# Optimization experiments

Measured on AMD Instinct MI355X. Metric: run time of the kernel, lower is better.

The kernel has to match this reference:

```python
import jax, jax.numpy as jnp
import numpy as np

N_HEADS = 4
HEAD_DIM = 64
NEG_SLOPE = 0.2
TIME_PE_DIM = 16


def time_pe(date):
    # TimePositionalEncoding: sin/cos features; 8 sin + 8 cos == pe_dim (16), no projection needed
    t = date.astype(jnp.float32) / 10000.0
    div = jnp.exp(jnp.arange(0, TIME_PE_DIM, 2, dtype=jnp.float32) * (-jnp.log(10000.0) / TIME_PE_DIM))
    arg = t[:, None] * div[None, :]  # [N, 8]
    return jnp.concatenate([jnp.sin(arg), jnp.cos(arg)], axis=-1)  # [N, 16]


def pearl_pe(x, edge_index, Wp, bp):
    # PEARL positional embedding approximated as mean-neighbor aggregation over the
    # union of all relations followed by a learned linear + tanh -> [N, 32]
    N = x.shape[0]
    src = edge_index[:, 0, :].reshape(-1)
    dst = edge_index[:, 1, :].reshape(-1)
    agg = jax.ops.segment_sum(x[src], dst, num_segments=N)
    deg = jax.ops.segment_sum(jnp.ones_like(dst, jnp.float32), dst, num_segments=N)
    agg = agg / jnp.maximum(deg, 1.0)[:, None]
    return jnp.tanh(agg @ Wp + bp)


def gatv2(x, src, dst, Wl, Wr, att, b):
    # GATv2 message passing for one edge type; dropout is identity (eval mode)
    N = x.shape[0]
    xl = (x @ Wl).reshape(N, N_HEADS, HEAD_DIM)
    xr = (x @ Wr).reshape(N, N_HEADS, HEAD_DIM)
    m = xl[src] + xr[dst]                                   # [E, H, C]
    e = jnp.sum(jax.nn.leaky_relu(m, NEG_SLOPE) * att, -1)  # [E, H]
    emax = jax.ops.segment_max(e, dst, num_segments=N)
    emax = jnp.where(jnp.isfinite(emax), emax, 0.0)
    ex = jnp.exp(e - emax[dst])
    denom = jax.ops.segment_sum(ex, dst, num_segments=N)
    alpha = ex / (denom[dst] + 1e-16)                       # segment softmax over in-edges
    out = jax.ops.segment_sum(xl[src] * alpha[..., None], dst, num_segments=N)
    return out.reshape(N, N_HEADS * HEAD_DIM) + b


def rel_agg(h_rel, W, b, a):
    # attention-weighted combination across relation outputs: h_rel [N, R, hidden]
    s = jnp.einsum('nrh,h->nr', jnp.tanh(h_rel @ W + b), a)
    w = jax.nn.softmax(s, axis=-1)
    return jnp.einsum('nr,nrh->nh', w, h_rel)


def gnn_layer(h, edge_index, Wl, Wr, att, b, aW, ab, aa):
    R = edge_index.shape[0]
    # HeteroConv aggr='sum': sum GATv2 outputs across the 5 relations
    conv_sum = gatv2(h, edge_index[0, 0], edge_index[0, 1], Wl[0], Wr[0], att[0], b[0])
    for r in range(1, R):
        conv_sum = conv_sum + gatv2(h, edge_index[r, 0], edge_index[r, 1], Wl[r], Wr[r], att[r], b[r])
    # original forward feeds conv_output['stock'] for every relation key (identical copies)
    h_rel = jnp.broadcast_to(conv_sum[:, None, :], (conv_sum.shape[0], R, conv_sum.shape[1]))
    h = rel_agg(h_rel, aW, ab, aa)
    return jax.nn.relu(h)  # dropout identity in eval


def reference(x, date_tensor, edge_index, pearl_W, pearl_b, Wl0, Wr0, att0, b0,
              Wl1, Wr1, att1, b1, aggW, aggb, agga, out_W1, out_b1, out_W2, out_b2):
    pe = pearl_pe(x, edge_index, pearl_W, pearl_b)          # [N, 32]
    tpe = time_pe(date_tensor)                              # [N, 16]
    h = jnp.concatenate([x, pe, tpe], axis=1)               # [N, 112]
    h = gnn_layer(h, edge_index, Wl0, Wr0, att0, b0, aggW[0], aggb[0], agga[0])
    h = gnn_layer(h, edge_index, Wl1, Wr1, att1, b1, aggW[1], aggb[1], agga[1])
    h = jax.nn.relu(h @ out_W1 + out_b1)
    return h @ out_W2 + out_b2                              # [N, 3]


def setup_inputs():
    key = jax.random.key(0)
    ks = jax.random.split(key, 20)
    N, E, R = 20000, 320000, 5
    IN, PE, HID = 64, 32, 256
    IN0 = IN + PE + TIME_PE_DIM  # 112

    def nrm(k, shp, sc=0.05):
        return jax.random.normal(k, shp, jnp.float32) * sc

    return {
        'x': jax.random.normal(ks[0], (N, IN), jnp.float32),
        'date_tensor': jax.random.randint(ks[1], (N,), 0, 20000, jnp.int32),
        'edge_index': jax.random.randint(ks[2], (R, 2, E), 0, N, jnp.int32),
        'pearl_W': nrm(ks[3], (IN, PE)),
        'pearl_b': jnp.zeros((PE,), jnp.float32),
        'Wl0': nrm(ks[4], (R, IN0, HID)),
        'Wr0': nrm(ks[5], (R, IN0, HID)),
        'att0': nrm(ks[6], (R, N_HEADS, HEAD_DIM)),
        'b0': jnp.zeros((R, HID), jnp.float32),
        'Wl1': nrm(ks[7], (R, HID, HID)),
        'Wr1': nrm(ks[8], (R, HID, HID)),
        'att1': nrm(ks[9], (R, N_HEADS, HEAD_DIM)),
        'b1': jnp.zeros((R, HID), jnp.float32),
        'aggW': nrm(ks[10], (2, HID, HID)),
        'aggb': jnp.zeros((2, HID), jnp.float32),
        'agga': nrm(ks[11], (2, HID)),
        'out_W1': nrm(ks[12], (HID, HID // 2)),
        'out_b1': jnp.zeros((HID // 2,), jnp.float32),
        'out_W2': nrm(ks[13], (HID // 2, 3)),
        'out_b2': jnp.zeros((3,), jnp.float32),
    }
```

## Files before the change

kernel.cpp:

```cpp
#include <hip/hip_runtime.h>
#include <math.h>

typedef __bf16 bf16x8 __attribute__((ext_vector_type(8)));
typedef float f32x4 __attribute__((ext_vector_type(4)));
typedef unsigned short u16x8 __attribute__((ext_vector_type(8)));

#define GLD16(src, dst)                                                        \
    __builtin_amdgcn_global_load_lds(                                          \
        (const __attribute__((address_space(1))) void*)(src),                  \
        (__attribute__((address_space(3))) void*)(dst), 16, 0, 0)

__device__ inline float bf2f(unsigned short u) {
    union { unsigned int i; float f; } c;
    c.i = ((unsigned int)u) << 16;
    return c.f;
}

template <int CTRL>
__device__ inline float dpp_add(float v) {
    int s = __builtin_amdgcn_update_dpp(0, __builtin_bit_cast(int, v), CTRL, 0xF, 0xF, true);
    return v + __builtin_bit_cast(float, s);
}


__global__ __launch_bounds__(256) void count_kernel(const int* __restrict__ ei,
                                                    int* __restrict__ cnt, int N, int E) {
    int idx = blockIdx.x * 256 + threadIdx.x;
    if (idx >= 5 * E) return;
    int r = idx / E;
    int e = idx - r * E;
    int dst = ei[(size_t)r * 2 * E + E + e];
    atomicAdd(&cnt[r * N + dst], 1);
}

__global__ __launch_bounds__(256) void scanA_kernel(const int* __restrict__ cnt,
                                                    int* __restrict__ off,
                                                    int* __restrict__ csums, int N, int NC) {
    int r = blockIdx.y, c = blockIdx.x, t = threadIdx.x;
    int idx0 = c * 1024 + t * 4;
    int v0 = (idx0 + 0 < N) ? cnt[r * N + idx0 + 0] : 0;
    int v1 = (idx0 + 1 < N) ? cnt[r * N + idx0 + 1] : 0;
    int v2 = (idx0 + 2 < N) ? cnt[r * N + idx0 + 2] : 0;
    int v3 = (idx0 + 3 < N) ? cnt[r * N + idx0 + 3] : 0;
    int ts = v0 + v1 + v2 + v3;
    __shared__ int sd[256];
    sd[t] = ts;
    __syncthreads();
    for (int s = 1; s < 256; s <<= 1) {
        int add = (t >= s) ? sd[t - s] : 0;
        __syncthreads();
        sd[t] += add;
        __syncthreads();
    }
    int excl = sd[t] - ts;
    size_t base = (size_t)r * (N + 1);
    if (idx0 + 0 < N) off[base + idx0 + 0] = excl;
    if (idx0 + 1 < N) off[base + idx0 + 1] = excl + v0;
    if (idx0 + 2 < N) off[base + idx0 + 2] = excl + v0 + v1;
    if (idx0 + 3 < N) off[base + idx0 + 3] = excl + v0 + v1 + v2;
    if (t == 255) csums[r * NC + c] = sd[255];
}

__global__ __launch_bounds__(64) void scanB_kernel(int* __restrict__ csums,
                                                   int* __restrict__ off, int N, int NC) {
    int r = threadIdx.x;
    if (r < 5) {
        int run = 0;
        for (int c = 0; c < NC; c++) {
            int t = csums[r * NC + c];
            csums[r * NC + c] = run;
            run += t;
        }
        off[(size_t)r * (N + 1) + N] = run;
    }
}

__global__ __launch_bounds__(256) void scanC_kernel(int* __restrict__ off,
                                                    const int* __restrict__ csums,
                                                    int* __restrict__ cur,
                                                    int N, int NC) {
    int r = blockIdx.y, c = blockIdx.x, t = threadIdx.x;
    int add = csums[r * NC + c];
    int idx0 = c * 1024 + t * 4;
    size_t base = (size_t)r * (N + 1);
#pragma unroll
    for (int j = 0; j < 4; j++)
        if (idx0 + j < N) {
            int v = off[base + idx0 + j] + add;
            off[base + idx0 + j] = v;
            cur[r * N + idx0 + j] = v;
        }
}

__global__ __launch_bounds__(256) void scatter_kernel(const int* __restrict__ ei,
                                                      int* __restrict__ cur,
                                                      unsigned short* __restrict__ srcs,
                                                      int N, int E) {
    int idx = blockIdx.x * 256 + threadIdx.x;
    if (idx >= 5 * E) return;
    int r = idx / E;
    int e = idx - r * E;
    int src = ei[(size_t)r * 2 * E + e];
    int dst = ei[(size_t)r * 2 * E + E + e];
    int pos = atomicAdd(&cur[r * N + dst], 1);
    srcs[(size_t)r * E + pos] = (unsigned short)src;
}


__global__ __launch_bounds__(256) void xcvt_kernel(const float* __restrict__ x,
                                                   unsigned short* __restrict__ xb, int total) {
    int idx = (blockIdx.x * 256 + threadIdx.x) * 4;
    if (idx >= total) return;
    float4 v = *(const float4*)(x + idx);
    __bf16 b0 = (__bf16)v.x, b1 = (__bf16)v.y, b2 = (__bf16)v.z, b3 = (__bf16)v.w;
    unsigned short* p = xb + idx;
    p[0] = *(unsigned short*)&b0;
    p[1] = *(unsigned short*)&b1;
    p[2] = *(unsigned short*)&b2;
    p[3] = *(unsigned short*)&b3;
}


__global__ __launch_bounds__(256) void pearl_h0_kernel(
    const float* __restrict__ x, const unsigned short* __restrict__ xb,
    const int* __restrict__ date,
    const int* __restrict__ off, const unsigned short* __restrict__ srcs,
    const float* __restrict__ pW, const float* __restrict__ pb,
    float* __restrict__ h0, int N, int E) {
    int lane = threadIdx.x & 63;
    int wid = blockIdx.x * 4 + (threadIdx.x >> 6);
    if (wid >= N) return;
    int n = __builtin_amdgcn_readfirstlane(wid);

    float acc = 0.f;
    int deg = 0;
    for (int r = 0; r < 5; r++) {
        int kb = off[(size_t)r * (N + 1) + n];
        int ke = off[(size_t)r * (N + 1) + n + 1];
        deg += ke - kb;
        const unsigned short* sp = srcs + (size_t)r * E;
        int k = kb;
        for (; k + 8 <= ke; k += 8) {
            int i0 = sp[k], i1 = sp[k + 1], i2 = sp[k + 2], i3 = sp[k + 3];
            int i4 = sp[k + 4], i5 = sp[k + 5], i6 = sp[k + 6], i7 = sp[k + 7];
            float a0 = bf2f(xb[(size_t)i0 * 64 + lane]);
            float a1 = bf2f(xb[(size_t)i1 * 64 + lane]);
            float a2 = bf2f(xb[(size_t)i2 * 64 + lane]);
            float a3 = bf2f(xb[(size_t)i3 * 64 + lane]);
            float a4 = bf2f(xb[(size_t)i4 * 64 + lane]);
            float a5 = bf2f(xb[(size_t)i5 * 64 + lane]);
            float a6 = bf2f(xb[(size_t)i6 * 64 + lane]);
            float a7 = bf2f(xb[(size_t)i7 * 64 + lane]);
            acc += ((a0 + a1) + (a2 + a3)) + ((a4 + a5) + (a6 + a7));
        }
        for (; k < ke; k++) acc += bf2f(xb[(size_t)sp[k] * 64 + lane]);
    }
    float an = acc / fmaxf((float)deg, 1.0f);

    float s = (lane < 32) ? pb[lane] : 0.f;
#pragma unroll 8
    for (int c = 0; c < 64; c++) {
        float av = __shfl(an, c, 64);
        if (lane < 32) s = fmaf(av, pW[c * 32 + lane], s);
    }

    h0[(size_t)n * 112 + lane] = x[(size_t)n * 64 + lane];
    if (lane < 32) h0[(size_t)n * 112 + 64 + lane] = tanhf(s);
    if (lane < 16) {
        float t = (float)date[n] / 10000.0f;
        int i = lane & 7;
        float dv = expf((float)(2 * i) * (-0.57564627324851148f));
        float arg = t * dv;
        h0[(size_t)n * 112 + 96 + lane] = (lane < 8) ? sinf(arg) : cosf(arg);
    }
}


__global__ __launch_bounds__(256) void pack_a_kernel(
    const float* __restrict__ A, __bf16* __restrict__ Ah, __bf16* __restrict__ Al,
    int M, int K, int Mp, int KT) {
    int KG = KT * 4;
    int idx = blockIdx.x * 256 + threadIdx.x;
    if (idx >= Mp * KG) return;
    int m = idx / KG, kgg = idx - m * KG;
    int kt = kgg >> 2, kg = kgg & 3;
    int k0 = kt * 32 + kg * 8;
    int mt = m >> 4, mr = m & 15;
    size_t out = (((size_t)mt * KT + kt) * 64 + kg * 16 + mr) * 8;
    bf16x8 hv, lv;
#pragma unroll
    for (int j = 0; j < 8; j++) {
        int k = k0 + j;
        float v = (m < M && k < K) ? A[(size_t)m * K + k] : 0.f;
        __bf16 h = (__bf16)v;
        hv[j] = h;
        lv[j] = (__bf16)(v - (float)h);
    }
    *(bf16x8*)(Ah + out) = hv;
    *(bf16x8*)(Al + out) = lv;
}


__global__ __launch_bounds__(256) void pack_w_kernel(
    const float* __restrict__ Wl0, const float* __restrict__ Wr0,
    const float* __restrict__ Wl1, const float* __restrict__ Wr1,
    const float* __restrict__ W1,
    __bf16* __restrict__ Wph, __bf16* __restrict__ Wpl) {
    const int S0 = 32768, S1 = 65536;
    int t = blockIdx.y;
    const float* W;
    int K, Nc, KT;
    size_t dst;
    if (t < 5)       { W = Wl0 + (size_t)t * 112 * 256;        K = 112; Nc = 256; KT = 4; dst = (size_t)t * S0; }
    else if (t < 10) { W = Wr0 + (size_t)(t - 5) * 112 * 256;  K = 112; Nc = 256; KT = 4; dst = 163840 + (size_t)(t - 5) * S0; }
    else if (t < 15) { W = Wl1 + (size_t)(t - 10) * 256 * 256; K = 256; Nc = 256; KT = 8; dst = 327680 + (size_t)(t - 10) * S1; }
    else if (t < 20) { W = Wr1 + (size_t)(t - 15) * 256 * 256; K = 256; Nc = 256; KT = 8; dst = 655360 + (size_t)(t - 15) * S1; }
    else             { W = W1;                                  K = 256; Nc = 128; KT = 8; dst = 983040; }
    int entries = (Nc / 16) * KT * 64;
    int idx = blockIdx.x * 256 + threadIdx.x;
    if (idx >= entries) return;
    int nt = idx / (KT * 64);
    int rem = idx - nt * (KT * 64);
    int kt = rem >> 6, lane = rem & 63;
    int kg = lane >> 4, nr = lane & 15;
    bf16x8 hv, lv;
#pragma unroll
    for (int j = 0; j < 8; j++) {
        int k = kt * 32 + kg * 8 + j;
        float v = (k < K) ? W[(size_t)k * Nc + nt * 16 + nr] : 0.f;
        __bf16 h = (__bf16)v;
        hv[j] = h;
        lv[j] = (__bf16)(v - (float)h);
    }
    *(bf16x8*)(Wph + dst + (size_t)idx * 8) = hv;
    *(bf16x8*)(Wpl + dst + (size_t)idx * 8) = lv;
}


__global__ __launch_bounds__(256) void gemm_mfma(
    const __bf16* __restrict__ Ah, const __bf16* __restrict__ Al,
    const __bf16* __restrict__ WLh, const __bf16* __restrict__ WLl,
    const __bf16* __restrict__ WRh, const __bf16* __restrict__ WRl,
    size_t strideB, void* __restrict__ Cl, void* __restrict__ Cr, size_t CstrideBytes,
    int M, int Nout, int KT, const float* __restrict__ bias, int do_relu,
    int npL, int npR, int out_bf16, int NYT, int per_bx) {
    int lin = blockIdx.x;
    int bx = lin / per_bx, rem = lin % per_bx;
    int by = rem % NYT; rem /= NYT;
    int side = rem & 1;
    int r = rem >> 1;

    const __bf16* Bh = (side ? WRh : WLh) + (size_t)r * strideB;
    const __bf16* Bl = (side ? WRl : WLl) + (size_t)r * strideB;
    char* C = (char*)(side ? Cr : Cl) + (size_t)r * CstrideBytes;
    int np = side ? npR : npL;

    __shared__ __bf16 sAh[8 * 512], sAl[8 * 512], sBh[8 * 512], sBl[8 * 512];

    int tid = threadIdx.x, lane = tid & 63, w = tid >> 6;
    int wr = w >> 1, wc = w & 1;

    f32x4 acc[4][4] = {};

    for (int kt = 0; kt < KT; ++kt) {
        int tl = w * 2;
        size_t a0 = ((size_t)(bx * 8 + tl) * KT + kt) * 512 + lane * 8;
        size_t a1 = ((size_t)(bx * 8 + tl + 1) * KT + kt) * 512 + lane * 8;
        size_t b0 = ((size_t)(by * 8 + tl) * KT + kt) * 512 + lane * 8;
        size_t b1 = ((size_t)(by * 8 + tl + 1) * KT + kt) * 512 + lane * 8;
        GLD16(Ah + a0, sAh + tl * 512);
        GLD16(Ah + a1, sAh + (tl + 1) * 512);
        GLD16(Bh + b0, sBh + tl * 512);
        GLD16(Bh + b1, sBh + (tl + 1) * 512);
        if (np >= 2) {
            GLD16(Al + a0, sAl + tl * 512);
            GLD16(Al + a1, sAl + (tl + 1) * 512);
        }
        if (np == 3) {
            GLD16(Bl + b0, sBl + tl * 512);
            GLD16(Bl + b1, sBl + (tl + 1) * 512);
        }
        __syncthreads();

        bf16x8 ah[4], al[4], bh[4], bl[4];
#pragma unroll
        for (int i = 0; i < 4; i++) {
            ah[i] = *(const bf16x8*)(sAh + (wr * 4 + i) * 512 + lane * 8);
            bh[i] = *(const bf16x8*)(sBh + (wc * 4 + i) * 512 + lane * 8);
        }
        if (np >= 2) {
#pragma unroll
            for (int i = 0; i < 4; i++)
                al[i] = *(const bf16x8*)(sAl + (wr * 4 + i) * 512 + lane * 8);
        }
        if (np == 3) {
#pragma unroll
            for (int i = 0; i < 4; i++)
                bl[i] = *(const bf16x8*)(sBl + (wc * 4 + i) * 512 + lane * 8);
        }
#pragma unroll
        for (int i = 0; i < 4; i++)
#pragma unroll
            for (int j = 0; j < 4; j++) {
                acc[i][j] = __builtin_amdgcn_mfma_f32_16x16x32_bf16(ah[i], bh[j], acc[i][j], 0, 0, 0);
                if (np >= 2)
                    acc[i][j] = __builtin_amdgcn_mfma_f32_16x16x32_bf16(al[i], bh[j], acc[i][j], 0, 0, 0);
                if (np == 3)
                    acc[i][j] = __builtin_amdgcn_mfma_f32_16x16x32_bf16(ah[i], bl[j], acc[i][j], 0, 0, 0);
            }
        __syncthreads();
    }

    int rb = bx * 128 + wr * 64, cb = by * 128 + wc * 64;
#pragma unroll
    for (int i = 0; i < 4; i++) {
#pragma unroll
        for (int j = 0; j < 4; j++) {
            int row0 = rb + i * 16 + (lane >> 4) * 4;
            int col = cb + j * 16 + (lane & 15);
            float bv = bias ? bias[col] : 0.f;
#pragma unroll
            for (int q = 0; q < 4; q++) {
                int row = row0 + q;
                if (row < M) {
                    float v = acc[i][j][q] + bv;
                    if (do_relu) v = fmaxf(v, 0.f);
                    if (out_bf16)
                        ((__bf16*)C)[(size_t)row * Nout + col] = (__bf16)v;
                    else
                        ((float*)C)[(size_t)row * Nout + col] = v;
                }
            }
        }
    }
}


__global__ __launch_bounds__(256) void gat5_kernel(
    const unsigned short* __restrict__ xl5, const unsigned short* __restrict__ xr5,
    const float* __restrict__ att,
    const int* __restrict__ csrOff,
    const unsigned short* __restrict__ csrSrc,
    float* __restrict__ conv, const float* __restrict__ bvec,
    int N, int E, int do_relu) {
    int lane = threadIdx.x & 63;
    int wid = blockIdx.x * 4 + (threadIdx.x >> 6);
    if (wid >= N) return;
    int n = __builtin_amdgcn_readfirstlane(wid);
    int e = lane >> 4;
    int sub = lane & 15;
    int cb = (sub >> 2) * 64 + (sub & 3) * 16;
    int wc = cb + e * 4;

    float4 cv = {0.f, 0.f, 0.f, 0.f};
#pragma unroll
    for (int r = 0; r < 5; r++) {
        float4 b = *(const float4*)(bvec + r * 256 + wc);
        cv.x += b.x; cv.y += b.y; cv.z += b.z; cv.w += b.w;
    }

    for (int r = 0; r < 5; r++) {
        const unsigned short* xl = xl5 + (size_t)r * N * 256;
        float rv[16], av6[16], av4[16];
        {
            const unsigned short* xrp = xr5 + ((size_t)r * N + n) * 256 + cb;
            u16x8 q0 = *(const u16x8*)(xrp);
            u16x8 q1 = *(const u16x8*)(xrp + 8);
#pragma unroll
            for (int j = 0; j < 8; j++) { rv[j] = bf2f(q0[j]); rv[8 + j] = bf2f(q1[j]); }
#pragma unroll
            for (int j = 0; j < 16; j += 4) {
                float4 a = *(const float4*)(att + r * 256 + cb + j);
                av6[j] = 0.6f * a.x; av6[j + 1] = 0.6f * a.y;
                av6[j + 2] = 0.6f * a.z; av6[j + 3] = 0.6f * a.w;
                av4[j] = 0.4f * a.x; av4[j + 1] = 0.4f * a.y;
                av4[j + 2] = 0.4f * a.z; av4[j + 3] = 0.4f * a.w;
            }
        }

        float d = 0.f;
        float A[16];
#pragma unroll
        for (int j = 0; j < 16; j++) A[j] = 0.f;

        const int* off = csrOff + (size_t)r * (N + 1);
        const unsigned short* sp = csrSrc + (size_t)r * E;
        int kb = off[n], ke = off[n + 1];
        if (kb < ke) {
            int kl = ke - 1;
            int ki = kb + e;
            int s = sp[(ki <= kl) ? ki : kl];
            float c[16];
            {
                const unsigned short* xp = xl + (size_t)s * 256 + cb;
                u16x8 q0 = *(const u16x8*)(xp);
                u16x8 q1 = *(const u16x8*)(xp + 8);
#pragma unroll
                for (int j = 0; j < 8; j++) { c[j] = bf2f(q0[j]); c[8 + j] = bf2f(q1[j]); }
            }
            for (int k = kb; k < ke; k += 4) {
                int kn = k + 4 + e;
                int sn = sp[(kn <= kl) ? kn : kl];
                const unsigned short* np_ = xl + (size_t)sn * 256 + cb;
                u16x8 n0 = *(const u16x8*)(np_);
                u16x8 n1 = *(const u16x8*)(np_ + 8);

                float pa = 0.f, pbv = 0.f;
#pragma unroll
                for (int j = 0; j < 16; j++) {
                    float t = c[j] + rv[j];
                    pa = fmaf(t, av6[j], pa);
                    pbv = fmaf(fabsf(t), av4[j], pbv);
                }
                float p = pa + pbv;
                p = dpp_add<0xB1>(p);
                p = dpp_add<0x4E>(p);
                bool valid = (k + e) < ke;
                float wg = valid ? __expf(p) : 0.f;
                d += wg;
#pragma unroll
                for (int j = 0; j < 16; j++) A[j] = fmaf(wg, c[j], A[j]);

#pragma unroll
                for (int j = 0; j < 8; j++) { c[j] = bf2f(n0[j]); c[8 + j] = bf2f(n1[j]); }
            }
        }

        d += __shfl_xor(d, 16, 64);
        d += __shfl_xor(d, 32, 64);
#pragma unroll
        for (int j = 0; j < 16; j++) {
            A[j] += __shfl_xor(A[j], 16, 64);
            A[j] += __shfl_xor(A[j], 32, 64);
        }

        float inv = 1.0f / (d + 1e-16f);
        cv.x = fmaf(A[e * 4 + 0], inv, cv.x);
        cv.y = fmaf(A[e * 4 + 1], inv, cv.y);
        cv.z = fmaf(A[e * 4 + 2], inv, cv.z);
        cv.w = fmaf(A[e * 4 + 3], inv, cv.w);
    }

    if (do_relu) {
        cv.x = fmaxf(cv.x, 0.f);
        cv.y = fmaxf(cv.y, 0.f);
        cv.z = fmaxf(cv.z, 0.f);
        cv.w = fmaxf(cv.w, 0.f);
    }
    *(float4*)(conv + (size_t)n * 256 + wc) = cv;
}


__global__ __launch_bounds__(256) void head_kernel(const float* __restrict__ hm,
                                                   const float* __restrict__ W2,
                                                   const float* __restrict__ b2,
                                                   float* __restrict__ out, int N) {
    int lane = threadIdx.x & 63;
    int wid = blockIdx.x * 4 + (threadIdx.x >> 6);
    if (wid >= N) return;
    int n = __builtin_amdgcn_readfirstlane(wid);
    float a0 = hm[(size_t)n * 128 + lane];
    float a1 = hm[(size_t)n * 128 + 64 + lane];
    float s0 = a0 * W2[lane * 3 + 0] + a1 * W2[(64 + lane) * 3 + 0];
    float s1 = a0 * W2[lane * 3 + 1] + a1 * W2[(64 + lane) * 3 + 1];
    float s2 = a0 * W2[lane * 3 + 2] + a1 * W2[(64 + lane) * 3 + 2];
#pragma unroll
    for (int sft = 1; sft < 64; sft <<= 1) {
        s0 += __shfl_xor(s0, sft, 64);
        s1 += __shfl_xor(s1, sft, 64);
        s2 += __shfl_xor(s2, sft, 64);
    }
    if (lane == 0) {
        out[(size_t)n * 3 + 0] = s0 + b2[0];
        out[(size_t)n * 3 + 1] = s1 + b2[1];
        out[(size_t)n * 3 + 2] = s2 + b2[2];
    }
}


extern "C" void kernel_launch(void* const* d_in, const int* in_sizes, int n_in,
                              void* d_out, int out_size, void* d_ws, size_t ws_size,
                              hipStream_t stream) {
    const float* x    = (const float*)d_in[0];
    const int* date   = (const int*)d_in[1];
    const int* ei     = (const int*)d_in[2];
    const float* pW   = (const float*)d_in[3];
    const float* pb   = (const float*)d_in[4];
    const float* Wl0  = (const float*)d_in[5];
    const float* Wr0  = (const float*)d_in[6];
    const float* att0 = (const float*)d_in[7];
    const float* b0   = (const float*)d_in[8];
    const float* Wl1  = (const float*)d_in[9];
    const float* Wr1  = (const float*)d_in[10];
    const float* att1 = (const float*)d_in[11];
    const float* b1   = (const float*)d_in[12];
    const float* outW1 = (const float*)d_in[16];
    const float* outb1 = (const float*)d_in[17];
    const float* outW2 = (const float*)d_in[18];
    const float* outb2 = (const float*)d_in[19];
    float* out = (float*)d_out;

    int N = in_sizes[0] / 64;
    int E = in_sizes[2] / 10;
    int Mp = ((N + 127) / 128) * 128;
    int MT = Mp / 128;
    int NC = (N + 1023) / 1024;

    char* ws = (char*)d_ws;
    size_t o = 0;
    auto alloc = [&](size_t bytes) -> char* {
        char* p = ws + o;
        o += (bytes + 255) & ~(size_t)255;
        return p;
    };
    int* cur               = (int*)alloc((size_t)5 * N * 4);
    int* csrOff            = (int*)alloc((size_t)5 * (N + 1) * 4);
    unsigned short* csrSrc = (unsigned short*)alloc((size_t)5 * E * 2);
    int* csums             = (int*)alloc((size_t)5 * NC * 4);
    unsigned short* xb16   = (unsigned short*)alloc((size_t)N * 64 * 2);
    float* h0              = (float*)alloc((size_t)N * 112 * 4);
    float* conv            = (float*)alloc((size_t)N * 256 * 4);
    unsigned short* xl5    = (unsigned short*)alloc((size_t)5 * N * 256 * 2);
    unsigned short* xr5    = (unsigned short*)alloc((size_t)5 * N * 256 * 2);
    __bf16* Aph            = (__bf16*)alloc((size_t)Mp * 256 * 2);
    __bf16* Apl            = (__bf16*)alloc((size_t)Mp * 256 * 2);
    __bf16* Wph            = (__bf16*)alloc((size_t)1015808 * 2);
    __bf16* Wpl            = (__bf16*)alloc((size_t)1015808 * 2);
    float* hmid            = (float*)xl5;
    (void)ws_size;

    const size_t S0 = 32768, S1 = 65536;
    const size_t oWl0 = 0, oWr0 = 163840, oWl1 = 327680, oWr1 = 655360, oW1 = 983040;
    size_t xstride = (size_t)N * 256 * 2;

    int totE = 5 * E;

    hipMemsetAsync(cur, 0, (size_t)5 * N * 4, stream);
    count_kernel<<<(totE + 255) / 256, 256, 0, stream>>>(ei, cur, N, E);
    scanA_kernel<<<dim3(NC, 5), 256, 0, stream>>>(cur, csrOff, csums, N, NC);
    scanB_kernel<<<1, 64, 0, stream>>>(csums, csrOff, N, NC);
    scanC_kernel<<<dim3(NC, 5), 256, 0, stream>>>(csrOff, csums, cur, N, NC);
    scatter_kernel<<<(totE + 255) / 256, 256, 0, stream>>>(ei, cur, csrSrc, N, E);

    xcvt_kernel<<<(N * 64 / 4 + 255) / 256, 256, 0, stream>>>(x, xb16, N * 64);
    pearl_h0_kernel<<<(N + 3) / 4, 256, 0, stream>>>(x, xb16, date, csrOff, csrSrc, pW, pb, h0, N, E);

    pack_w_kernel<<<dim3(32, 21, 1), 256, 0, stream>>>(Wl0, Wr0, Wl1, Wr1, outW1, Wph, Wpl);

    pack_a_kernel<<<(Mp * 16 + 255) / 256, 256, 0, stream>>>(h0, Aph, Apl, N, 112, Mp, 4);
    gemm_mfma<<<MT * 20, 256, 0, stream>>>(
        Aph, Apl, Wph + oWl0, Wpl + oWl0, Wph + oWr0, Wpl + oWr0, S0,
        xl5, xr5, xstride, N, 256, 4, nullptr, 0, 2, 1, 1, 2, 20);
    gat5_kernel<<<(N + 3) / 4, 256, 0, stream>>>(xl5, xr5, att0, csrOff, csrSrc,
                                                 conv, b0, N, E, 1);

    pack_a_kernel<<<(Mp * 32 + 255) / 256, 256, 0, stream>>>(conv, Aph, Apl, N, 256, Mp, 8);
    gemm_mfma<<<MT * 20, 256, 0, stream>>>(
        Aph, Apl, Wph + oWl1, Wpl + oWl1, Wph + oWr1, Wpl + oWr1, S1,
        xl5, xr5, xstride, N, 256, 8, nullptr, 0, 2, 1, 1, 2, 20);
    gat5_kernel<<<(N + 3) / 4, 256, 0, stream>>>(xl5, xr5, att1, csrOff, csrSrc,
                                                 conv, b1, N, E, 1);

    pack_a_kernel<<<(Mp * 32 + 255) / 256, 256, 0, stream>>>(conv, Aph, Apl, N, 256, Mp, 8);
    gemm_mfma<<<MT, 256, 0, stream>>>(
        Aph, Apl, Wph + oW1, Wpl + oW1, Wph + oW1, Wpl + oW1, 0,
        hmid, hmid, 0, N, 128, 8, outb1, 1, 3, 3, 0, 1, 1);
    head_kernel<<<(N + 3) / 4, 256, 0, stream>>>(hmid, outW2, outb2, out, N);
}
```

Baseline: 822.0 us.

## Cut GAT kernel registers via reduce-scatter shuffles and merged attention coefficients

```diff
diff --git a/kernel.cpp b/kernel.cpp
--- a/kernel.cpp
+++ b/kernel.cpp
@@ -140,18 +140,24 @@
         deg += ke - kb;
         const unsigned short* sp = srcs + (size_t)r * E;
         int k = kb;
-        for (; k + 8 <= ke; k += 8) {
+        for (; k + 16 <= ke; k += 16) {
+            int ix[16];
+#pragma unroll
+            for (int j = 0; j < 16; j++) ix[j] = sp[k + j];
+            float a[16];
+#pragma unroll
+            for (int j = 0; j < 16; j++) a[j] = bf2f(xb[(size_t)ix[j] * 64 + lane]);
+            float s0 = ((a[0] + a[1]) + (a[2] + a[3])) + ((a[4] + a[5]) + (a[6] + a[7]));
+            float s1 = ((a[8] + a[9]) + (a[10] + a[11])) + ((a[12] + a[13]) + (a[14] + a[15]));
+            acc += s0 + s1;
+        }
+        for (; k + 4 <= ke; k += 4) {
             int i0 = sp[k], i1 = sp[k + 1], i2 = sp[k + 2], i3 = sp[k + 3];
-            int i4 = sp[k + 4], i5 = sp[k + 5], i6 = sp[k + 6], i7 = sp[k + 7];
             float a0 = bf2f(xb[(size_t)i0 * 64 + lane]);
             float a1 = bf2f(xb[(size_t)i1 * 64 + lane]);
             float a2 = bf2f(xb[(size_t)i2 * 64 + lane]);
             float a3 = bf2f(xb[(size_t)i3 * 64 + lane]);
-            float a4 = bf2f(xb[(size_t)i4 * 64 + lane]);
-            float a5 = bf2f(xb[(size_t)i5 * 64 + lane]);
-            float a6 = bf2f(xb[(size_t)i6 * 64 + lane]);
-            float a7 = bf2f(xb[(size_t)i7 * 64 + lane]);
-            acc += ((a0 + a1) + (a2 + a3)) + ((a4 + a5) + (a6 + a7));
+            acc += (a0 + a1) + (a2 + a3);
         }
         for (; k < ke; k++) acc += bf2f(xb[(size_t)sp[k] * 64 + lane]);
     }
@@ -336,7 +342,7 @@
 }
 
 
-__global__ __launch_bounds__(256) void gat5_kernel(
+__global__ __launch_bounds__(256, 8) void gat5_kernel(
     const unsigned short* __restrict__ xl5, const unsigned short* __restrict__ xr5,
     const float* __restrict__ att,
     const int* __restrict__ csrOff,
@@ -361,7 +367,7 @@
 
     for (int r = 0; r < 5; r++) {
         const unsigned short* xl = xl5 + (size_t)r * N * 256;
-        float rv[16], av6[16], av4[16];
+        float rv[16], av6[16];
         {
             const unsigned short* xrp = xr5 + ((size_t)r * N + n) * 256 + cb;
             u16x8 q0 = *(const u16x8*)(xrp);
@@ -373,8 +379,6 @@
                 float4 a = *(const float4*)(att + r * 256 + cb + j);
                 av6[j] = 0.6f * a.x; av6[j + 1] = 0.6f * a.y;
                 av6[j + 2] = 0.6f * a.z; av6[j + 3] = 0.6f * a.w;
-                av4[j] = 0.4f * a.x; av4[j + 1] = 0.4f * a.y;
-                av4[j + 2] = 0.4f * a.z; av4[j + 3] = 0.4f * a.w;
             }
         }
 
@@ -410,9 +414,9 @@
                 for (int j = 0; j < 16; j++) {
                     float t = c[j] + rv[j];
                     pa = fmaf(t, av6[j], pa);
-                    pbv = fmaf(fabsf(t), av4[j], pbv);
+                    pbv = fmaf(fabsf(t), av6[j], pbv);
                 }
-                float p = pa + pbv;
+                float p = fmaf(0.66666667f, pbv, pa);
                 p = dpp_add<0xB1>(p);
                 p = dpp_add<0x4E>(p);
                 bool valid = (k + e) < ke;
@@ -426,19 +430,30 @@
             }
         }
 
+        bool hi2 = (e & 2) != 0;
+        float S1[8];
+#pragma unroll
+        for (int i = 0; i < 8; i++) {
+            float keep = hi2 ? A[8 + i] : A[i];
+            float send = hi2 ? A[i] : A[8 + i];
+            S1[i] = keep + __shfl_xor(send, 32, 64);
+        }
+        bool hi1 = (e & 1) != 0;
+        float S2[4];
+#pragma unroll
+        for (int i = 0; i < 4; i++) {
+            float keep = hi1 ? S1[4 + i] : S1[i];
+            float send = hi1 ? S1[i] : S1[4 + i];
+            S2[i] = keep + __shfl_xor(send, 16, 64);
+        }
         d += __shfl_xor(d, 16, 64);
         d += __shfl_xor(d, 32, 64);
-#pragma unroll
-        for (int j = 0; j < 16; j++) {
-            A[j] += __shfl_xor(A[j], 16, 64);
-            A[j] += __shfl_xor(A[j], 32, 64);
-        }
 
         float inv = 1.0f / (d + 1e-16f);
-        cv.x = fmaf(A[e * 4 + 0], inv, cv.x);
-        cv.y = fmaf(A[e * 4 + 1], inv, cv.y);
-        cv.z = fmaf(A[e * 4 + 2], inv, cv.z);
-        cv.w = fmaf(A[e * 4 + 3], inv, cv.w);
+        cv.x = fmaf(S2[0], inv, cv.x);
+        cv.y = fmaf(S2[1], inv, cv.y);
+        cv.z = fmaf(S2[2], inv, cv.z);
+        cv.w = fmaf(S2[3], inv, cv.w);
     }
 
     if (do_relu) {
```

Result: slower. 1.314 ms (+59.8%).
